# Performance work log

Hardware: AMD Instinct MI355X
Metric: run time of the kernel (lower is better)

Reference implementation:

```python
import jax, jax.numpy as jnp
import numpy as np

N_NODES = 75000
N_EDGES = 1200000
DIM = 64


def setup_inputs() -> dict:
    key = jax.random.key(0)
    ks = jax.random.split(key, 9)
    d_u = jax.random.normal(ks[0], (N_NODES, DIM), dtype=jnp.float32)
    p_u = jax.random.normal(ks[1], (N_NODES, DIM), dtype=jnp.float32)
    s = 1.0 / np.sqrt(DIM)
    w_q = jax.random.normal(ks[2], (DIM, DIM), dtype=jnp.float32) * s
    w_k = jax.random.normal(ks[3], (DIM, DIM), dtype=jnp.float32) * s
    w_v = jax.random.normal(ks[4], (DIM, DIM), dtype=jnp.float32) * s
    e1 = jax.random.normal(ks[5], (DIM,), dtype=jnp.float32) * s
    e2 = jax.random.normal(ks[6], (DIM,), dtype=jnp.float32) * s
    src = jax.random.randint(ks[7], (N_EDGES,), 0, N_NODES, dtype=jnp.int32)
    dst = jax.random.randint(ks[8], (N_EDGES,), 0, N_NODES, dtype=jnp.int32)
    return {"d_u": d_u, "p_u": p_u, "w_q": w_q, "w_k": w_k, "w_v": w_v,
            "e1": e1, "e2": e2, "src": src, "dst": dst}


def reference(d_u, p_u, w_q, w_k, w_v, e1, e2, src, dst):
    n_nodes = d_u.shape[0]
    # per-node edge scores: e1(w_k(p_u)) on src side, e2(w_q(d_u)) on dst side
    h_src = (p_u @ w_k.T) @ e1            # [N]
    h_dst = (d_u @ w_q.T) @ e2            # [N]
    # apply_edges(u_add_v): c_e = h_src[u] + h_dst[v], shape [E]
    c = h_src[src] + h_dst[dst]
    # EdgeWeightNorm(norm='right'): divide by sum of incoming edge weights at dst
    denom = jax.ops.segment_sum(c, dst, num_segments=n_nodes)  # [N]
    c = c / denom[dst]
    # update_all(u_mul_e, sum): messages w_v(p_u)[u] * c_e, summed at dst
    wv = p_u @ w_v.T                      # [N, D]
    msg = wv[src] * c[:, None]            # [E, D]
    out = jax.ops.segment_sum(msg, dst, num_segments=n_nodes)  # [N, D]
    return out
```

## Files before the change

### kernel.cpp

```cpp
#include <hip/hip_runtime.h>

#define N_NODES 75000
#define N_EDGES 1200000
#define DIM 64
#define SCAN_BLK 1024
#define N_SCAN_BLKS ((N_NODES + SCAN_BLK - 1) / SCAN_BLK)

__global__ void vec_precompute(const float* __restrict__ w_q,
                               const float* __restrict__ w_k,
                               const float* __restrict__ e1,
                               const float* __restrict__ e2,
                               double* __restrict__ a,
                               double* __restrict__ b) {
    int t = threadIdx.x;
    if (t < DIM) {
        double s = 0.0;
        #pragma unroll
        for (int j = 0; j < DIM; ++j) s += (double)e1[j] * (double)w_k[j * DIM + t];
        a[t] = s;
    } else if (t < 2 * DIM) {
        int d = t - DIM;
        double s = 0.0;
        #pragma unroll
        for (int j = 0; j < DIM; ++j) s += (double)e2[j] * (double)w_q[j * DIM + d];
        b[d] = s;
    }
}

__global__ __launch_bounds__(256) void node_kernel(
    const float* __restrict__ d_u, const float* __restrict__ p_u,
    const float* __restrict__ w_v,
    const double* __restrict__ a_vec, const double* __restrict__ b_vec,
    double* __restrict__ h_src, double* __restrict__ h_dst,
    float* __restrict__ wv_out) {
    int i = blockIdx.x * 256 + threadIdx.x;
    if (i >= N_NODES) return;

    float p[DIM];
    const float4* prow = (const float4*)(p_u + (size_t)i * DIM);
    #pragma unroll
    for (int k = 0; k < DIM / 4; ++k) {
        float4 v = prow[k];
        p[4 * k + 0] = v.x; p[4 * k + 1] = v.y;
        p[4 * k + 2] = v.z; p[4 * k + 3] = v.w;
    }

    double hs = 0.0;
    #pragma unroll
    for (int d = 0; d < DIM; ++d) hs += (double)p[d] * a_vec[d];
    h_src[i] = hs;

    double hd = 0.0;
    const float4* drow = (const float4*)(d_u + (size_t)i * DIM);
    #pragma unroll
    for (int k = 0; k < DIM / 4; ++k) {
        float4 v = drow[k];
        hd += (double)v.x * b_vec[4 * k + 0] + (double)v.y * b_vec[4 * k + 1] +
              (double)v.z * b_vec[4 * k + 2] + (double)v.w * b_vec[4 * k + 3];
    }
    h_dst[i] = hd;

    float* wvrow = wv_out + (size_t)i * DIM;
    #pragma unroll
    for (int j = 0; j < DIM; j += 4) {
        float a0 = 0.f, a1 = 0.f, a2 = 0.f, a3 = 0.f;
        #pragma unroll
        for (int d = 0; d < DIM; ++d) {
            float pd = p[d];
            a0 += w_v[(j + 0) * DIM + d] * pd;
            a1 += w_v[(j + 1) * DIM + d] * pd;
            a2 += w_v[(j + 2) * DIM + d] * pd;
            a3 += w_v[(j + 3) * DIM + d] * pd;
        }
        float4 r; r.x = a0; r.y = a1; r.z = a2; r.w = a3;
        ((float4*)wvrow)[j >> 2] = r;
    }
}

__global__ __launch_bounds__(256) void hist_kernel(
    const int* __restrict__ dst, int* __restrict__ cnt,
    int* __restrict__ rank) {
    int e = blockIdx.x * 256 + threadIdx.x;
    if (e >= N_EDGES) return;
    rank[e] = atomicAdd(&cnt[dst[e]], 1);
}

__global__ __launch_bounds__(SCAN_BLK) void scan1_kernel(
    const int* __restrict__ cnt, int* __restrict__ row,
    int* __restrict__ bsum) {
    __shared__ int sh[SCAN_BLK];
    int tid = threadIdx.x;
    int i = blockIdx.x * SCAN_BLK + tid;
    int v = (i < N_NODES) ? cnt[i] : 0;
    sh[tid] = v;
    __syncthreads();
    for (int off = 1; off < SCAN_BLK; off <<= 1) {
        int t = (tid >= off) ? sh[tid - off] : 0;
        __syncthreads();
        sh[tid] += t;
        __syncthreads();
    }
    if (i < N_NODES) row[i] = sh[tid] - v;
    if (tid == SCAN_BLK - 1) bsum[blockIdx.x] = sh[tid];
}

__global__ __launch_bounds__(256) void scan23_kernel(
    int* __restrict__ row, const int* __restrict__ bsum) {
    __shared__ int pref[N_SCAN_BLKS];
    int tid = threadIdx.x;
    if (tid == 0) {
        int run = 0;
        #pragma unroll 8
        for (int k = 0; k < N_SCAN_BLKS; ++k) { pref[k] = run; run += bsum[k]; }
    }
    __syncthreads();
    int i = blockIdx.x * 256 + tid;
    if (i >= N_NODES) return;
    row[i] += pref[i / SCAN_BLK];
}

__global__ __launch_bounds__(256) void build_kernel(
    const int* __restrict__ src, const int* __restrict__ dst,
    const int* __restrict__ row, const int* __restrict__ rank,
    int* __restrict__ csr_src) {
    int e = blockIdx.x * 256 + threadIdx.x;
    if (e >= N_EDGES) return;
    int pos = row[dst[e]] + rank[e];
    csr_src[pos] = src[e];
}

__global__ __launch_bounds__(256) void node_gather(
    const int* __restrict__ row, const int* __restrict__ cnt,
    const int* __restrict__ csr_src,
    const double* __restrict__ h_src, const double* __restrict__ h_dst,
    const float* __restrict__ wv, float* __restrict__ out) {
    int gtid = blockIdx.x * 256 + threadIdx.x;
    int node = gtid >> 6;
    int lane = threadIdx.x & 63;
    if (node >= N_NODES) return;

    int start = row[node];
    int deg = cnt[node];
    double hd = h_dst[node];

    if (deg <= 64) {
        int s0 = 0;
        double c0 = 0.0;
        if (lane < deg) {
            s0 = csr_src[start + lane];
            c0 = h_src[s0] + hd;
        }
        double r = c0;
        #pragma unroll
        for (int off = 32; off > 0; off >>= 1) r += __shfl_xor(r, off, 64);
        double inv = 1.0 / r;
        float cf0 = (lane < deg) ? (float)(c0 * inv) : 0.f;

        int g = lane >> 4;
        int q = lane & 15;
        int tmax = (deg + 3) >> 2;
        float ax = 0.f, ay = 0.f, az = 0.f, aw = 0.f;
        for (int t = 0; t < tmax; ++t) {
            int idx = 4 * t + g;
            int s = __shfl(s0, idx, 64);
            float cf = __shfl(cf0, idx, 64);
            const float4* rowp = (const float4*)(wv + (size_t)s * DIM);
            float4 w = rowp[q];
            ax += w.x * cf;
            ay += w.y * cf;
            az += w.z * cf;
            aw += w.w * cf;
        }
        ax += __shfl_xor(ax, 16, 64);
        ay += __shfl_xor(ay, 16, 64);
        az += __shfl_xor(az, 16, 64);
        aw += __shfl_xor(aw, 16, 64);
        ax += __shfl_xor(ax, 32, 64);
        ay += __shfl_xor(ay, 32, 64);
        az += __shfl_xor(az, 32, 64);
        aw += __shfl_xor(aw, 32, 64);
        if (lane < 16) {
            float4 st; st.x = ax; st.y = ay; st.z = az; st.w = aw;
            ((float4*)(out + (size_t)node * DIM))[q] = st;
        }
    } else {
        double denom = 0.0;
        for (int base = 0; base < deg; base += 64) {
            int m = deg - base; if (m > 64) m = 64;
            double c = 0.0;
            if (lane < m) {
                int s = csr_src[start + base + lane];
                c = h_src[s] + hd;
            }
            #pragma unroll
            for (int off = 32; off > 0; off >>= 1) c += __shfl_xor(c, off, 64);
            denom += c;
        }
        double inv = 1.0 / denom;
        float acc = 0.f;
        for (int base = 0; base < deg; base += 64) {
            int m = deg - base; if (m > 64) m = 64;
            int s1 = 0; float cf1 = 0.f;
            if (lane < m) {
                s1 = csr_src[start + base + lane];
                cf1 = (float)((h_src[s1] + hd) * inv);
            }
            for (int j = 0; j < m; ++j) {
                int s = __shfl(s1, j, 64);
                float cf = __shfl(cf1, j, 64);
                acc += wv[(size_t)s * DIM + lane] * cf;
            }
        }
        out[(size_t)node * DIM + lane] = acc;
    }
}

extern "C" void kernel_launch(void* const* d_in, const int* in_sizes, int n_in,
                              void* d_out, int out_size, void* d_ws, size_t ws_size,
                              hipStream_t stream) {
    const float* d_u = (const float*)d_in[0];
    const float* p_u = (const float*)d_in[1];
    const float* w_q = (const float*)d_in[2];
    const float* w_k = (const float*)d_in[3];
    const float* w_v = (const float*)d_in[4];
    const float* e1  = (const float*)d_in[5];
    const float* e2  = (const float*)d_in[6];
    const int*   src = (const int*)d_in[7];
    const int*   dst = (const int*)d_in[8];
    float* out = (float*)d_out;

    double* a      = (double*)d_ws;
    double* b      = a + DIM;
    double* h_src  = b + DIM;
    double* h_dst  = h_src + N_NODES;
    float*  wv     = (float*)(h_dst + N_NODES);
    int*    cnt    = (int*)(wv + (size_t)N_NODES * DIM);
    int*    row    = cnt + N_NODES;
    int*    bsum   = row + N_NODES;
    int*    rank   = bsum + 128;
    int*    csr_src= rank + N_EDGES;

    vec_precompute<<<1, 128, 0, stream>>>(w_q, w_k, e1, e2, a, b);

    hipMemsetAsync(cnt, 0, sizeof(int) * N_NODES, stream);

    hist_kernel<<<(N_EDGES + 255) / 256, 256, 0, stream>>>(dst, cnt, rank);

    node_kernel<<<(N_NODES + 255) / 256, 256, 0, stream>>>(
        d_u, p_u, w_v, a, b, h_src, h_dst, wv);

    scan1_kernel<<<N_SCAN_BLKS, SCAN_BLK, 0, stream>>>(cnt, row, bsum);
    scan23_kernel<<<(N_NODES + 255) / 256, 256, 0, stream>>>(row, bsum);

    build_kernel<<<(N_EDGES + 255) / 256, 256, 0, stream>>>(
        src, dst, row, rank, csr_src);

    node_gather<<<(N_NODES * 64 + 255) / 256, 256, 0, stream>>>(
        row, cnt, csr_src, h_src, h_dst, wv, out);
}
```

Measured before the change: 276.6 us.

## Split node kernel into h-score and w_v projection kernels with 4 threads per node

Result: slower. 399.1 us (+44.3%).

```diff
diff --git a/kernel.cpp b/kernel.cpp
--- a/kernel.cpp
+++ b/kernel.cpp
@@ -27,27 +27,21 @@
     }
 }
 
-__global__ __launch_bounds__(256) void node_kernel(
+__global__ __launch_bounds__(256, 4) void h_kernel(
     const float* __restrict__ d_u, const float* __restrict__ p_u,
-    const float* __restrict__ w_v,
     const double* __restrict__ a_vec, const double* __restrict__ b_vec,
-    double* __restrict__ h_src, double* __restrict__ h_dst,
-    float* __restrict__ wv_out) {
+    double* __restrict__ h_src, double* __restrict__ h_dst) {
     int i = blockIdx.x * 256 + threadIdx.x;
     if (i >= N_NODES) return;
 
-    float p[DIM];
+    double hs = 0.0;
     const float4* prow = (const float4*)(p_u + (size_t)i * DIM);
     #pragma unroll
     for (int k = 0; k < DIM / 4; ++k) {
         float4 v = prow[k];
-        p[4 * k + 0] = v.x; p[4 * k + 1] = v.y;
-        p[4 * k + 2] = v.z; p[4 * k + 3] = v.w;
-    }
-
-    double hs = 0.0;
-    #pragma unroll
-    for (int d = 0; d < DIM; ++d) hs += (double)p[d] * a_vec[d];
+        hs += (double)v.x * a_vec[4 * k + 0] + (double)v.y * a_vec[4 * k + 1] +
+              (double)v.z * a_vec[4 * k + 2] + (double)v.w * a_vec[4 * k + 3];
+    }
     h_src[i] = hs;
 
     double hd = 0.0;
@@ -59,21 +53,48 @@
               (double)v.z * b_vec[4 * k + 2] + (double)v.w * b_vec[4 * k + 3];
     }
     h_dst[i] = hd;
-
-    float* wvrow = wv_out + (size_t)i * DIM;
-    #pragma unroll
-    for (int j = 0; j < DIM; j += 4) {
-        float a0 = 0.f, a1 = 0.f, a2 = 0.f, a3 = 0.f;
-        #pragma unroll
-        for (int d = 0; d < DIM; ++d) {
-            float pd = p[d];
-            a0 += w_v[(j + 0) * DIM + d] * pd;
-            a1 += w_v[(j + 1) * DIM + d] * pd;
-            a2 += w_v[(j + 2) * DIM + d] * pd;
-            a3 += w_v[(j + 3) * DIM + d] * pd;
-        }
-        float4 r; r.x = a0; r.y = a1; r.z = a2; r.w = a3;
-        ((float4*)wvrow)[j >> 2] = r;
+}
+
+
+__global__ __launch_bounds__(256, 4) void wv_kernel(
+    const float* __restrict__ p_u, const float* __restrict__ w_v,
+    float* __restrict__ wv_out) {
+    int t = blockIdx.x * 256 + threadIdx.x;
+    int i = t >> 2;
+    int g = t & 3;
+    if (i >= N_NODES) return;
+
+    const float4* prow = (const float4*)(p_u + (size_t)i * DIM);
+    float acc[16];
+    #pragma unroll
+    for (int jj = 0; jj < 16; ++jj) acc[jj] = 0.f;
+
+    #pragma unroll
+    for (int kc = 0; kc < 4; ++kc) {
+        float4 pc[4];
+        #pragma unroll
+        for (int k = 0; k < 4; ++k) pc[k] = prow[kc * 4 + k];
+        #pragma unroll
+        for (int jj = 0; jj < 16; ++jj) {
+            int j = g * 16 + jj;
+            const float4* wrow = (const float4*)(w_v + (size_t)j * DIM + kc * 16);
+            float s = 0.f;
+            #pragma unroll
+            for (int k = 0; k < 4; ++k) {
+                float4 w = wrow[k];
+                s += w.x * pc[k].x + w.y * pc[k].y + w.z * pc[k].z + w.w * pc[k].w;
+            }
+            acc[jj] += s;
+        }
+    }
+
+    float4* orow = (float4*)(wv_out + (size_t)i * DIM + g * 16);
+    #pragma unroll
+    for (int jj = 0; jj < 4; ++jj) {
+        float4 st;
+        st.x = acc[4 * jj + 0]; st.y = acc[4 * jj + 1];
+        st.z = acc[4 * jj + 2]; st.w = acc[4 * jj + 3];
+        orow[jj] = st;
     }
 }
 
@@ -246,8 +267,10 @@
 
     hist_kernel<<<(N_EDGES + 255) / 256, 256, 0, stream>>>(dst, cnt, rank);
 
-    node_kernel<<<(N_NODES + 255) / 256, 256, 0, stream>>>(
-        d_u, p_u, w_v, a, b, h_src, h_dst, wv);
+    h_kernel<<<(N_NODES + 255) / 256, 256, 0, stream>>>(
+        d_u, p_u, a, b, h_src, h_dst);
+
+    wv_kernel<<<(N_NODES * 4 + 255) / 256, 256, 0, stream>>>(p_u, w_v, wv);
 
     scan1_kernel<<<N_SCAN_BLKS, SCAN_BLK, 0, stream>>>(cnt, row, bsum);
     scan23_kernel<<<(N_NODES + 255) / 256, 256, 0, stream>>>(row, bsum);
```

## Process one node per wavefront with register-resident w_v row per lane

Applied to the files above, without the earlier changes.

Result: slower. 306.9 us (+11.0%).

```diff
diff --git a/kernel.cpp b/kernel.cpp
--- a/kernel.cpp
+++ b/kernel.cpp
@@ -27,53 +27,48 @@
     }
 }
 
-__global__ __launch_bounds__(256) void node_kernel(
+__global__ __launch_bounds__(256, 4) void node_wave(
     const float* __restrict__ d_u, const float* __restrict__ p_u,
     const float* __restrict__ w_v,
     const double* __restrict__ a_vec, const double* __restrict__ b_vec,
     double* __restrict__ h_src, double* __restrict__ h_dst,
     float* __restrict__ wv_out) {
-    int i = blockIdx.x * 256 + threadIdx.x;
-    if (i >= N_NODES) return;
-
-    float p[DIM];
-    const float4* prow = (const float4*)(p_u + (size_t)i * DIM);
+    int lane = threadIdx.x & 63;
+    int wave = (blockIdx.x * 256 + threadIdx.x) >> 6;
+    int nwaves = gridDim.x * 4;
+
+    float w[DIM];
+    const float4* wr = (const float4*)(w_v + (size_t)lane * DIM);
     #pragma unroll
     for (int k = 0; k < DIM / 4; ++k) {
-        float4 v = prow[k];
-        p[4 * k + 0] = v.x; p[4 * k + 1] = v.y;
-        p[4 * k + 2] = v.z; p[4 * k + 3] = v.w;
-    }
-
-    double hs = 0.0;
-    #pragma unroll
-    for (int d = 0; d < DIM; ++d) hs += (double)p[d] * a_vec[d];
-    h_src[i] = hs;
-
-    double hd = 0.0;
-    const float4* drow = (const float4*)(d_u + (size_t)i * DIM);
-    #pragma unroll
-    for (int k = 0; k < DIM / 4; ++k) {
-        float4 v = drow[k];
-        hd += (double)v.x * b_vec[4 * k + 0] + (double)v.y * b_vec[4 * k + 1] +
-              (double)v.z * b_vec[4 * k + 2] + (double)v.w * b_vec[4 * k + 3];
-    }
-    h_dst[i] = hd;
-
-    float* wvrow = wv_out + (size_t)i * DIM;
-    #pragma unroll
-    for (int j = 0; j < DIM; j += 4) {
+        float4 v = wr[k];
+        w[4 * k + 0] = v.x; w[4 * k + 1] = v.y;
+        w[4 * k + 2] = v.z; w[4 * k + 3] = v.w;
+    }
+    double al = a_vec[lane];
+    double bl = b_vec[lane];
+
+    for (int i = wave; i < N_NODES; i += nwaves) {
+        float pl = p_u[(size_t)i * DIM + lane];
+        float dl = d_u[(size_t)i * DIM + lane];
+
+        double hs = (double)pl * al;
+        #pragma unroll
+        for (int off = 32; off > 0; off >>= 1) hs += __shfl_xor(hs, off, 64);
+        double hd = (double)dl * bl;
+        #pragma unroll
+        for (int off = 32; off > 0; off >>= 1) hd += __shfl_xor(hd, off, 64);
+        if (lane == 0) { h_src[i] = hs; h_dst[i] = hd; }
+
         float a0 = 0.f, a1 = 0.f, a2 = 0.f, a3 = 0.f;
         #pragma unroll
-        for (int d = 0; d < DIM; ++d) {
-            float pd = p[d];
-            a0 += w_v[(j + 0) * DIM + d] * pd;
-            a1 += w_v[(j + 1) * DIM + d] * pd;
-            a2 += w_v[(j + 2) * DIM + d] * pd;
-            a3 += w_v[(j + 3) * DIM + d] * pd;
-        }
-        float4 r; r.x = a0; r.y = a1; r.z = a2; r.w = a3;
-        ((float4*)wvrow)[j >> 2] = r;
+        for (int d = 0; d < DIM; d += 4) {
+            a0 += w[d + 0] * __shfl(pl, d + 0, 64);
+            a1 += w[d + 1] * __shfl(pl, d + 1, 64);
+            a2 += w[d + 2] * __shfl(pl, d + 2, 64);
+            a3 += w[d + 3] * __shfl(pl, d + 3, 64);
+        }
+        wv_out[(size_t)i * DIM + lane] = (a0 + a1) + (a2 + a3);
     }
 }
 
@@ -246,7 +241,7 @@
 
     hist_kernel<<<(N_EDGES + 255) / 256, 256, 0, stream>>>(dst, cnt, rank);
 
-    node_kernel<<<(N_NODES + 255) / 256, 256, 0, stream>>>(
+    node_wave<<<1024, 256, 0, stream>>>(
         d_u, p_u, w_v, a, b, h_src, h_dst, wv);
 
     scan1_kernel<<<N_SCAN_BLKS, SCAN_BLK, 0, stream>>>(cnt, row, bsum);
```
